# Performance work log

Measured on AMD Instinct MI355X. Metric: run time of the kernel, lower is better.

## Reference

```python
import jax, jax.numpy as jnp
import numpy as np

C_IN, C_HID, N_HEADS = 64, 8, 8
INF, EPS, LN_EPS = 1000000000.0, 1e-10, 1e-5


def setup_inputs() -> dict:
    key = jax.random.key(0)
    ks = jax.random.split(key, 8)
    B, S, R = 1, 2048, 512  # batch, n_seq, n_res
    m = jax.random.normal(ks[0], (B, S, R, C_IN), dtype=jnp.float32)
    mask = jnp.ones((B, S, R), dtype=jnp.float32)
    sc = 1.0 / np.sqrt(C_IN)
    return {
        "m": m,
        "mask": mask,
        "ln_w": jnp.ones((C_IN,), jnp.float32),
        "ln_b": jnp.zeros((C_IN,), jnp.float32),
        "wq": jax.random.normal(ks[1], (C_IN, N_HEADS * C_HID), jnp.float32) * sc,
        "wk": jax.random.normal(ks[2], (C_IN, C_HID), jnp.float32) * sc,
        "wv": jax.random.normal(ks[3], (C_IN, C_HID), jnp.float32) * sc,
        "wg": jax.random.normal(ks[4], (C_IN, N_HEADS * C_HID), jnp.float32) * sc,
        "bg": jnp.ones((N_HEADS * C_HID,), jnp.float32),  # gating bias init to 1
        "wo": jax.random.normal(ks[5], (N_HEADS * C_HID, C_IN), jnp.float32) * sc,
        "bo": jnp.zeros((C_IN,), jnp.float32),
    }


def _layernorm(x, w, b):
    mu = jnp.mean(x, axis=-1, keepdims=True)
    var = jnp.mean(jnp.square(x - mu), axis=-1, keepdims=True)
    return (x - mu) * jax.lax.rsqrt(var + LN_EPS) * w + b


def reference(m, mask, ln_w, ln_b, wq, wk, wv, wg, bg, wo, bo):
    # m: [B, S, R, C]; attend over the MSA (S) axis per residue column.
    x = jnp.swapaxes(m, -2, -3)        # [B, R, S, C]
    msk = jnp.swapaxes(mask, -1, -2)   # [B, R, S]
    x = _layernorm(x, ln_w, ln_b)

    # mean-pooled query over the sequence axis
    q_pool = jnp.sum(x * msk[..., None], axis=-2) / (
        jnp.sum(msk, axis=-1)[..., None] + EPS)           # [B, R, C]
    q = (q_pool @ wq) * (C_HID ** -0.5)                    # [B, R, H*Ch]
    q = q.reshape(*q.shape[:-1], N_HEADS, C_HID)           # [B, R, H, Ch]

    k = x @ wk                                             # [B, R, S, Ch]
    v = x @ wv                                             # [B, R, S, Ch]

    bias = INF * (msk - 1.0)                               # [B, R, S]
    logits = jnp.einsum('brhc,brsc->brhs', q, k) + bias[..., None, :]
    a = jax.nn.softmax(logits, axis=-1)                    # [B, R, H, S]
    o = jnp.einsum('brhs,brsc->brhc', a, v)                # [B, R, H, Ch]

    g = jax.nn.sigmoid(x @ wg + bg)                        # [B, R, S, H*Ch]
    g = g.reshape(*g.shape[:-1], N_HEADS, C_HID)           # [B, R, S, H, Ch]
    o = o[..., None, :, :] * g                             # [B, R, S, H, Ch]
    o = o.reshape(*o.shape[:-2], N_HEADS * C_HID)          # [B, R, S, H*Ch]
    out = o @ wo + bo                                      # [B, R, S, C]
    return jnp.swapaxes(out, -2, -3)                       # [B, S, R, C]
```

## Files before the change

### kernel.cpp

```cpp
#include <hip/hip_runtime.h>
#include <hip/hip_bf16.h>

#define S_DIM 2048
#define R_DIM 512
#define C_DIM 64
#define LN_EPSF 1e-5f
#define EPSF 1e-10f
#define INFF 1000000000.0f

typedef __attribute__((ext_vector_type(4))) float f32x4;
typedef __attribute__((ext_vector_type(8))) short bf16x8;

__device__ __forceinline__ int SWZ(int row, int cb) {
  return row * 128 + (cb ^ ((row & 7) << 4));
}

__device__ __forceinline__ float wave_sum64(float v) {
#pragma unroll
  for (int m = 1; m < 64; m <<= 1) v += __shfl_xor(v, m, 64);
  return v;
}

__device__ __forceinline__ float bf2f(unsigned short u) {
  return __uint_as_float(((unsigned int)u) << 16);
}

__global__ __launch_bounds__(256) void kW(const float* __restrict__ wg,
                                          const float* __restrict__ wo,
                                          __hip_bfloat16* __restrict__ wgT,
                                          __hip_bfloat16* __restrict__ woT) {
  const float* src = blockIdx.x ? wo : wg;
  __hip_bfloat16* dst = blockIdx.x ? woT : wgT;
  for (int idx = threadIdx.x; idx < 4096; idx += 256) {
    const int n = idx >> 6, k = idx & 63;
    dst[idx] = __float2bfloat16(src[k * 64 + n]);
  }
}

template <bool STORE_X>
__global__ __launch_bounds__(256) void kA(
    const float* __restrict__ m_in, const float* __restrict__ mask,
    const float* __restrict__ ln_w, const float* __restrict__ ln_b,
    const float* __restrict__ wk, const float* __restrict__ wv,
    __hip_bfloat16* __restrict__ x_ws, __hip_bfloat16* __restrict__ k_ws,
    __hip_bfloat16* __restrict__ v_ws, float* __restrict__ qnum,
    float* __restrict__ msum) {
  const int tid = threadIdx.x;
  const int w = tid >> 6;
  const int lane = tid & 63;
  const int r = blockIdx.x & (R_DIM - 1);
  const int chunk = blockIdx.x >> 9;
  const int s_base = chunk * 32;

  const float lw = ln_w[lane];
  const float lb = ln_b[lane];

  const int j = lane & 15;
  const int q4 = lane >> 4;
  const int jj = j & 7;
  const float* wmat = (j < 8) ? wk : wv;
  float wreg[16];
#pragma unroll
  for (int cc = 0; cc < 16; ++cc) wreg[cc] = wmat[(q4 * 16 + cc) * 8 + jj];

  float qacc = 0.f;
  float macc = 0.f;

  for (int it = 0; it < 8; ++it) {
    const int s = s_base + it * 4 + w;
    const size_t pos = (size_t)s * R_DIM + r;
    const float xv = m_in[pos * 64 + lane];
    const float mk = mask[pos];
    const float mu = wave_sum64(xv) * (1.f / 64.f);
    const float d = xv - mu;
    const float var = wave_sum64(d * d) * (1.f / 64.f);
    const float xn = fmaf(d * rsqrtf(var + LN_EPSF), lw, lb);

    qacc = fmaf(xn, mk, qacc);
    macc += mk;

    if (STORE_X) x_ws[pos * 64 + lane] = __float2bfloat16(xn);

    float acc = 0.f;
#pragma unroll
    for (int cc = 0; cc < 16; ++cc) {
      const float xc = __shfl(xn, q4 * 16 + cc, 64);
      acc = fmaf(xc, wreg[cc], acc);
    }
    acc += __shfl_xor(acc, 16, 64);
    acc += __shfl_xor(acc, 32, 64);
    if (lane < 16) {
      const __hip_bfloat16 hb = __float2bfloat16(acc);
      const size_t kvb = ((size_t)r * S_DIM + s) * 8 + jj;
      if (lane < 8) k_ws[kvb] = hb; else v_ws[kvb] = hb;
    }
  }

  __shared__ float qsm[4][64];
  __shared__ float mssm[4];
  qsm[w][lane] = qacc;
  if (lane == 0) mssm[w] = macc;
  __syncthreads();
  if (w == 0) {
    const float t = qsm[0][lane] + qsm[1][lane] + qsm[2][lane] + qsm[3][lane];
    atomicAdd(&qnum[r * 64 + lane], t);
    if (lane == 0) atomicAdd(&msum[r], mssm[0] + mssm[1] + mssm[2] + mssm[3]);
  }
}

__global__ __launch_bounds__(256) void kB(
    const float* __restrict__ qnum, const float* __restrict__ msum,
    const float* __restrict__ mask, const float* __restrict__ wq,
    const __hip_bfloat16* __restrict__ k_ws,
    const __hip_bfloat16* __restrict__ v_ws, float* __restrict__ o_ws) {
  const int r = blockIdx.x;
  const int tid = threadIdx.x;
  __shared__ float qp_sm[64];
  __shared__ float q_sm[64];
  if (tid < 64) qp_sm[tid] = qnum[r * 64 + tid] / (msum[r] + EPSF);
  __syncthreads();
  if (tid < 64) {
    float a = 0.f;
#pragma unroll
    for (int c = 0; c < 64; ++c) a = fmaf(qp_sm[c], wq[c * 64 + tid], a);
    q_sm[tid] = a * 0.35355339059327373f;
  }
  __syncthreads();

  const int w = tid >> 6;
  const int lane = tid & 63;
  const int h0 = w * 2;
  float qh0[8], qh1[8];
#pragma unroll
  for (int ch = 0; ch < 8; ++ch) {
    qh0[ch] = q_sm[h0 * 8 + ch];
    qh1[ch] = q_sm[h0 * 8 + 8 + ch];
  }
  float m0 = -1e30f, l0 = 0.f, m1 = -1e30f, l1 = 0.f;
  float a0[8], a1[8];
#pragma unroll
  for (int ch = 0; ch < 8; ++ch) { a0[ch] = 0.f; a1[ch] = 0.f; }

  for (int it = 0; it < 32; ++it) {
    const int s = it * 64 + lane;
    const size_t kb = ((size_t)r * S_DIM + s) * 8;
    union { uint4 u; unsigned short us[8]; } ku, vu;
    ku.u = *reinterpret_cast<const uint4*>(&k_ws[kb]);
    vu.u = *reinterpret_cast<const uint4*>(&v_ws[kb]);
    const float bias = INFF * (mask[(size_t)s * R_DIM + r] - 1.f);
    float lg0 = bias, lg1 = bias;
#pragma unroll
    for (int ch = 0; ch < 8; ++ch) {
      const float kc = bf2f(ku.us[ch]);
      lg0 = fmaf(qh0[ch], kc, lg0);
      lg1 = fmaf(qh1[ch], kc, lg1);
    }
    const float nm0 = fmaxf(m0, lg0);
    const float c0 = __expf(m0 - nm0);
    const float p0 = __expf(lg0 - nm0);
    const float nm1 = fmaxf(m1, lg1);
    const float c1 = __expf(m1 - nm1);
    const float p1 = __expf(lg1 - nm1);
    l0 = fmaf(l0, c0, p0); m0 = nm0;
    l1 = fmaf(l1, c1, p1); m1 = nm1;
#pragma unroll
    for (int ch = 0; ch < 8; ++ch) {
      const float vc = bf2f(vu.us[ch]);
      a0[ch] = fmaf(a0[ch], c0, p0 * vc);
      a1[ch] = fmaf(a1[ch], c1, p1 * vc);
    }
  }
#pragma unroll
  for (int msk = 1; msk < 64; msk <<= 1) {
    {
      const float om = __shfl_xor(m0, msk, 64);
      const float ol = __shfl_xor(l0, msk, 64);
      const float nm = fmaxf(m0, om);
      const float ca = __expf(m0 - nm);
      const float cb = __expf(om - nm);
      l0 = l0 * ca + ol * cb;
#pragma unroll
      for (int ch = 0; ch < 8; ++ch) {
        const float oa = __shfl_xor(a0[ch], msk, 64);
        a0[ch] = a0[ch] * ca + oa * cb;
      }
      m0 = nm;
    }
    {
      const float om = __shfl_xor(m1, msk, 64);
      const float ol = __shfl_xor(l1, msk, 64);
      const float nm = fmaxf(m1, om);
      const float ca = __expf(m1 - nm);
      const float cb = __expf(om - nm);
      l1 = l1 * ca + ol * cb;
#pragma unroll
      for (int ch = 0; ch < 8; ++ch) {
        const float oa = __shfl_xor(a1[ch], msk, 64);
        a1[ch] = a1[ch] * ca + oa * cb;
      }
      m1 = nm;
    }
  }
  const float inv0 = 1.f / l0;
  const float inv1 = 1.f / l1;
#pragma unroll
  for (int ch = 0; ch < 8; ++ch) {
    if (lane == ch)     o_ws[r * 64 + h0 * 8 + ch]       = a0[ch] * inv0;
    if (lane == 8 + ch) o_ws[r * 64 + (h0 + 1) * 8 + ch] = a1[ch] * inv1;
  }
}

__global__ __launch_bounds__(256) void kC_mfma(
    const __hip_bfloat16* __restrict__ x_ws, const float* __restrict__ o_ws,
    const __hip_bfloat16* __restrict__ wgT, const __hip_bfloat16* __restrict__ woT,
    const float* __restrict__ bg, const float* __restrict__ bo,
    float* __restrict__ out) {
  __shared__ __align__(16) unsigned char smem[32768];
  unsigned char* xsm  = smem;
  unsigned char* wg_s = smem + 16384;
  unsigned char* wo_s = smem + 24576;
  const int t = threadIdx.x;
  const int w = t >> 6;
  const int l = t & 63;
  const size_t P0 = (size_t)blockIdx.x * 128;

  {
    const uint4* sg = (const uint4*)wgT;
    const uint4* so = (const uint4*)woT;
#pragma unroll
    for (int pp = 0; pp < 2; ++pp) {
      const int idx = pp * 256 + t;
      const int row = idx >> 3;
      const int cb = (idx & 7) * 16;
      *(uint4*)(wg_s + SWZ(row, cb)) = sg[idx];
      *(uint4*)(wo_s + SWZ(row, cb)) = so[idx];
    }
  }
  {
    const uint4* sx = (const uint4*)(x_ws + P0 * 64);
#pragma unroll
    for (int pp = 0; pp < 4; ++pp) {
      const int idx = pp * 256 + t;
      const int row = idx >> 3;
      const int cb = (idx & 7) * 16;
      *(uint4*)(xsm + SWZ(row, cb)) = sx[idx];
    }
  }
  __syncthreads();

  const int woff = w * 32;
  const int lrow = l & 15;
  const int g16 = l >> 4;

  f32x4 acc[2][4] = {};
#pragma unroll
  for (int ks = 0; ks < 2; ++ks) {
    bf16x8 a[2], b[4];
#pragma unroll
    for (int mb = 0; mb < 2; ++mb)
      a[mb] = *(const bf16x8*)(xsm + SWZ(woff + mb * 16 + lrow, ks * 64 + g16 * 16));
#pragma unroll
    for (int nb = 0; nb < 4; ++nb)
      b[nb] = *(const bf16x8*)(wg_s + SWZ(nb * 16 + lrow, ks * 64 + g16 * 16));
#pragma unroll
    for (int mb = 0; mb < 2; ++mb)
#pragma unroll
      for (int nb = 0; nb < 4; ++nb)
        acc[mb][nb] = __builtin_amdgcn_mfma_f32_16x16x32_bf16(a[mb], b[nb], acc[mb][nb], 0, 0, 0);
  }
  __syncthreads();

  const int r0 = (int)(P0 & (R_DIM - 1));
#pragma unroll
  for (int nb = 0; nb < 4; ++nb) {
    const int col = nb * 16 + lrow;
    const float bgv = bg[col];
#pragma unroll
    for (int mb = 0; mb < 2; ++mb) {
#pragma unroll
      for (int i = 0; i < 4; ++i) {
        const int row = woff + mb * 16 + g16 * 4 + i;
        const float gv = 1.f / (1.f + __expf(-(acc[mb][nb][i] + bgv)));
        const float og = gv * o_ws[(r0 + row) * 64 + col];
        *(__hip_bfloat16*)(xsm + SWZ(row, col * 2)) = __float2bfloat16(og);
      }
    }
  }
  __syncthreads();

  f32x4 acc2[2][4] = {};
#pragma unroll
  for (int ks = 0; ks < 2; ++ks) {
    bf16x8 a[2], b[4];
#pragma unroll
    for (int mb = 0; mb < 2; ++mb)
      a[mb] = *(const bf16x8*)(xsm + SWZ(woff + mb * 16 + lrow, ks * 64 + g16 * 16));
#pragma unroll
    for (int nb = 0; nb < 4; ++nb)
      b[nb] = *(const bf16x8*)(wo_s + SWZ(nb * 16 + lrow, ks * 64 + g16 * 16));
#pragma unroll
    for (int mb = 0; mb < 2; ++mb)
#pragma unroll
      for (int nb = 0; nb < 4; ++nb)
        acc2[mb][nb] = __builtin_amdgcn_mfma_f32_16x16x32_bf16(a[mb], b[nb], acc2[mb][nb], 0, 0, 0);
  }

#pragma unroll
  for (int nb = 0; nb < 4; ++nb) {
    const int col = nb * 16 + lrow;
    const float bov = bo[col];
#pragma unroll
    for (int mb = 0; mb < 2; ++mb)
#pragma unroll
      for (int i = 0; i < 4; ++i) {
        const int row = woff + mb * 16 + g16 * 4 + i;
        out[(P0 + row) * 64 + col] = acc2[mb][nb][i] + bov;
      }
  }
}

template <bool USE_X>
__global__ __launch_bounds__(256) void kC(
    const __hip_bfloat16* __restrict__ x_ws, const float* __restrict__ m_in,
    const float* __restrict__ ln_w, const float* __restrict__ ln_b,
    const float* __restrict__ o_ws, const float* __restrict__ wg,
    const float* __restrict__ bg, const float* __restrict__ wo,
    const float* __restrict__ bo, float* __restrict__ out) {
  const int tid = threadIdx.x;
  const int w = tid >> 6;
  const int lane = tid & 63;
  const size_t p0 = ((size_t)blockIdx.x * 4 + w) * 4;
  __shared__ float xsm[4][4][64];
  __shared__ float ogsm[4][4][64];

  if (USE_X) {
#pragma unroll
    for (int pp = 0; pp < 4; ++pp)
      xsm[w][pp][lane] = __bfloat162float(x_ws[(p0 + pp) * 64 + lane]);
  } else {
    const float lw = ln_w[lane];
    const float lb = ln_b[lane];
#pragma unroll
    for (int pp = 0; pp < 4; ++pp) {
      const float xv = m_in[(p0 + pp) * 64 + lane];
      const float mu = wave_sum64(xv) * (1.f / 64.f);
      const float d = xv - mu;
      const float var = wave_sum64(d * d) * (1.f / 64.f);
      xsm[w][pp][lane] = fmaf(d * rsqrtf(var + LN_EPSF), lw, lb);
    }
  }
  __syncthreads();

  float acc[4];
  const float bgv = bg[lane];
#pragma unroll
  for (int pp = 0; pp < 4; ++pp) acc[pp] = bgv;
#pragma unroll 4
  for (int c4 = 0; c4 < 16; ++c4) {
    const float wv0 = wg[(c4 * 4 + 0) * 64 + lane];
    const float wv1 = wg[(c4 * 4 + 1) * 64 + lane];
    const float wv2 = wg[(c4 * 4 + 2) * 64 + lane];
    const float wv3 = wg[(c4 * 4 + 3) * 64 + lane];
#pragma unroll
    for (int pp = 0; pp < 4; ++pp) {
      const float4 xq = *reinterpret_cast<const float4*>(&xsm[w][pp][c4 * 4]);
      acc[pp] = fmaf(xq.x, wv0, acc[pp]);
      acc[pp] = fmaf(xq.y, wv1, acc[pp]);
      acc[pp] = fmaf(xq.z, wv2, acc[pp]);
      acc[pp] = fmaf(xq.w, wv3, acc[pp]);
    }
  }
  const int rr = (int)(p0 & (R_DIM - 1));
#pragma unroll
  for (int pp = 0; pp < 4; ++pp) {
    const float g = 1.f / (1.f + __expf(-acc[pp]));
    ogsm[w][pp][lane] = g * o_ws[(rr + pp) * 64 + lane];
  }
  __syncthreads();

  float acc2[4];
  const float bov = bo[lane];
#pragma unroll
  for (int pp = 0; pp < 4; ++pp) acc2[pp] = bov;
#pragma unroll 4
  for (int j4 = 0; j4 < 16; ++j4) {
    const float wv0 = wo[(j4 * 4 + 0) * 64 + lane];
    const float wv1 = wo[(j4 * 4 + 1) * 64 + lane];
    const float wv2 = wo[(j4 * 4 + 2) * 64 + lane];
    const float wv3 = wo[(j4 * 4 + 3) * 64 + lane];
#pragma unroll
    for (int pp = 0; pp < 4; ++pp) {
      const float4 oq = *reinterpret_cast<const float4*>(&ogsm[w][pp][j4 * 4]);
      acc2[pp] = fmaf(oq.x, wv0, acc2[pp]);
      acc2[pp] = fmaf(oq.y, wv1, acc2[pp]);
      acc2[pp] = fmaf(oq.z, wv2, acc2[pp]);
      acc2[pp] = fmaf(oq.w, wv3, acc2[pp]);
    }
  }
#pragma unroll
  for (int pp = 0; pp < 4; ++pp) out[(p0 + pp) * 64 + lane] = acc2[pp];
}

extern "C" void kernel_launch(void* const* d_in, const int* in_sizes, int n_in,
                              void* d_out, int out_size, void* d_ws,
                              size_t ws_size, hipStream_t stream) {
  (void)in_sizes; (void)n_in; (void)out_size;
  const float* m_in = (const float*)d_in[0];
  const float* mask = (const float*)d_in[1];
  const float* ln_w = (const float*)d_in[2];
  const float* ln_b = (const float*)d_in[3];
  const float* wq   = (const float*)d_in[4];
  const float* wk   = (const float*)d_in[5];
  const float* wv   = (const float*)d_in[6];
  const float* wg   = (const float*)d_in[7];
  const float* bg   = (const float*)d_in[8];
  const float* wo   = (const float*)d_in[9];
  const float* bo   = (const float*)d_in[10];
  float* out = (float*)d_out;
  char* ws = (char*)d_ws;

  const size_t X_BYTES  = (size_t)S_DIM * R_DIM * 64 * 2;
  const size_t KV_BYTES = (size_t)S_DIM * R_DIM * 8 * 2;
  const size_t QN_BYTES = (size_t)R_DIM * 64 * 4;
  const size_t MS_BYTES = (size_t)R_DIM * 4;
  const size_t O_BYTES  = (size_t)R_DIM * 64 * 4;
  const size_t WT_BYTES = 64 * 64 * 2;

  const size_t need_big =
      X_BYTES + 2 * KV_BYTES + QN_BYTES + MS_BYTES + O_BYTES + 2 * WT_BYTES;
  const bool use_x = ws_size >= need_big;

  size_t off = use_x ? X_BYTES : 0;
  __hip_bfloat16* x_ws = (__hip_bfloat16*)ws;
  __hip_bfloat16* k_ws = (__hip_bfloat16*)(ws + off); off += KV_BYTES;
  __hip_bfloat16* v_ws = (__hip_bfloat16*)(ws + off); off += KV_BYTES;
  float* qnum = (float*)(ws + off); off += QN_BYTES;
  float* msum = (float*)(ws + off); off += MS_BYTES;
  float* o_ws = (float*)(ws + off); off += O_BYTES;
  __hip_bfloat16* wgT = (__hip_bfloat16*)(ws + off); off += WT_BYTES;
  __hip_bfloat16* woT = (__hip_bfloat16*)(ws + off);

  hipMemsetAsync(qnum, 0, QN_BYTES + MS_BYTES, stream);

  const int gridA = R_DIM * (S_DIM / 32);
  if (use_x) {
    kW<<<2, 256, 0, stream>>>(wg, wo, wgT, woT);
    kA<true><<<gridA, 256, 0, stream>>>(m_in, mask, ln_w, ln_b, wk, wv, x_ws,
                                        k_ws, v_ws, qnum, msum);
    kB<<<R_DIM, 256, 0, stream>>>(qnum, msum, mask, wq, k_ws, v_ws, o_ws);
    const int gridC = (S_DIM * R_DIM) / 128;
    kC_mfma<<<gridC, 256, 0, stream>>>(x_ws, o_ws, wgT, woT, bg, bo, out);
  } else {
    kA<false><<<gridA, 256, 0, stream>>>(m_in, mask, ln_w, ln_b, wk, wv, x_ws,
                                         k_ws, v_ws, qnum, msum);
    kB<<<R_DIM, 256, 0, stream>>>(qnum, msum, mask, wq, k_ws, v_ws, o_ws);
    const int gridC = (S_DIM * R_DIM) / 16;
    kC<false><<<gridC, 256, 0, stream>>>(nullptr, m_in, ln_w, ln_b, o_ws, wg,
                                         bg, wo, bo, out);
  }
}
```

Baseline: 829.1 us.

## Rewrite LayerNorm/KV projection kernel with MFMA and 32-residue tiles

Replaces the per-position wave-level LayerNorm and shuffle-based K/V projection with a new kernel in which each block handles a 32-residue by 32-sequence tile. Two threads share a row and hold 32 floats each, so the LN statistics need only one shuffle. The K/V projection now runs as bf16 MFMA on a swizzled LDS tile, with K/V outputs staged in LDS and written as contiguous 16-byte stores. Query-pool accumulation switches from per-block LDS reduction plus atomics to per-thread register accumulators with many more global atomics. This adds register pressure (launch bounds set to 3 blocks per CU) and a larger atomic count in exchange for vectorised loads, far fewer shuffles and coalesced writes.

```diff
diff --git a/kernel.cpp b/kernel.cpp
--- a/kernel.cpp
+++ b/kernel.cpp
@@ -27,13 +27,180 @@
 
 __global__ __launch_bounds__(256) void kW(const float* __restrict__ wg,
                                           const float* __restrict__ wo,
+                                          const float* __restrict__ wk,
+                                          const float* __restrict__ wv,
                                           __hip_bfloat16* __restrict__ wgT,
-                                          __hip_bfloat16* __restrict__ woT) {
-  const float* src = blockIdx.x ? wo : wg;
-  __hip_bfloat16* dst = blockIdx.x ? woT : wgT;
-  for (int idx = threadIdx.x; idx < 4096; idx += 256) {
-    const int n = idx >> 6, k = idx & 63;
-    dst[idx] = __float2bfloat16(src[k * 64 + n]);
+                                          __hip_bfloat16* __restrict__ woT,
+                                          __hip_bfloat16* __restrict__ wkvT) {
+  if (blockIdx.x < 2) {
+    const float* src = blockIdx.x ? wo : wg;
+    __hip_bfloat16* dst = blockIdx.x ? woT : wgT;
+    for (int idx = threadIdx.x; idx < 4096; idx += 256) {
+      const int n = idx >> 6, k = idx & 63;
+      dst[idx] = __float2bfloat16(src[k * 64 + n]);
+    }
+  } else {
+    for (int idx = threadIdx.x; idx < 1024; idx += 256) {
+      const int n = idx >> 6, c = idx & 63;
+      const float v = (n < 8) ? wk[c * 8 + n] : wv[c * 8 + (n - 8)];
+      wkvT[idx] = __float2bfloat16(v);
+    }
+  }
+}
+
+template <bool STORE_X>
+__global__ __launch_bounds__(256, 3) void kA2(
+    const float* __restrict__ m_in, const float* __restrict__ mask,
+    const float* __restrict__ ln_w, const float* __restrict__ ln_b,
+    const __hip_bfloat16* __restrict__ wkvT, __hip_bfloat16* __restrict__ x_ws,
+    __hip_bfloat16* __restrict__ k_ws, __hip_bfloat16* __restrict__ v_ws,
+    float* __restrict__ qnum, float* __restrict__ msum) {
+  __shared__ __align__(16) unsigned char xsm[16384];
+  __shared__ __align__(16) unsigned char wkv_s[2048];
+  __shared__ __align__(16) unsigned char kvb[32768];
+
+  const int t = threadIdx.x;
+  const int w = t >> 6;
+  const int l = t & 63;
+  const int row = (t >> 1) & 31;
+  const int half = t & 1;
+  const int r0 = (blockIdx.x & 15) * 32;
+  const int s0 = (blockIdx.x >> 4) * 32;
+
+  if (t < 128) {
+    const uint4* src = (const uint4*)wkvT;
+    *(uint4*)(wkv_s + SWZ(t >> 3, (t & 7) * 16)) = src[t];
+  }
+
+  float lw[32], lb[32];
+  {
+    const float4* pw = (const float4*)(ln_w + half * 32);
+    const float4* pb = (const float4*)(ln_b + half * 32);
+#pragma unroll
+    for (int k = 0; k < 8; ++k) {
+      const float4 a = pw[k], b = pb[k];
+      lw[k * 4 + 0] = a.x; lw[k * 4 + 1] = a.y; lw[k * 4 + 2] = a.z; lw[k * 4 + 3] = a.w;
+      lb[k * 4 + 0] = b.x; lb[k * 4 + 1] = b.y; lb[k * 4 + 2] = b.z; lb[k * 4 + 3] = b.w;
+    }
+  }
+
+  float qacc[32];
+#pragma unroll
+  for (int j = 0; j < 32; ++j) qacc[j] = 0.f;
+  float macc = 0.f;
+
+  const int lrow = l & 15;
+  const int g16 = l >> 4;
+  unsigned char* xtile = xsm + w * 4096;
+
+  __syncthreads();
+
+  for (int it = 0; it < 8; ++it) {
+    const int s = s0 + it * 4 + w;
+    const size_t pos = (size_t)s * R_DIM + r0 + row;
+
+    float x[32];
+    {
+      const float4* pm = (const float4*)(m_in + pos * 64 + half * 32);
+#pragma unroll
+      for (int k = 0; k < 8; ++k) {
+        const float4 v4 = pm[k];
+        x[k * 4 + 0] = v4.x; x[k * 4 + 1] = v4.y;
+        x[k * 4 + 2] = v4.z; x[k * 4 + 3] = v4.w;
+      }
+    }
+    const float mk = mask[pos];
+
+    float sum = 0.f, sq = 0.f;
+#pragma unroll
+    for (int j = 0; j < 32; ++j) {
+      sum += x[j];
+      sq = fmaf(x[j], x[j], sq);
+    }
+    sum += __shfl_xor(sum, 1, 64);
+    sq += __shfl_xor(sq, 1, 64);
+    const float mu = sum * (1.f / 64.f);
+    const float var = sq * (1.f / 64.f) - mu * mu;
+    const float rs = rsqrtf(var + LN_EPSF);
+    const float nbias = -mu * rs;
+
+    unsigned int pk[16];
+#pragma unroll
+    for (int j = 0; j < 16; ++j) {
+      const float xn0 = fmaf(fmaf(x[2 * j], rs, nbias), lw[2 * j], lb[2 * j]);
+      const float xn1 = fmaf(fmaf(x[2 * j + 1], rs, nbias), lw[2 * j + 1], lb[2 * j + 1]);
+      qacc[2 * j] = fmaf(xn0, mk, qacc[2 * j]);
+      qacc[2 * j + 1] = fmaf(xn1, mk, qacc[2 * j + 1]);
+      const unsigned u0 = __bfloat16_as_ushort(__float2bfloat16(xn0));
+      const unsigned u1 = __bfloat16_as_ushort(__float2bfloat16(xn1));
+      pk[j] = u0 | (u1 << 16);
+    }
+    macc += mk;
+
+    if (STORE_X) {
+      uint4* dst = (uint4*)(x_ws + pos * 64 + half * 32);
+      const uint4* s4 = (const uint4*)pk;
+#pragma unroll
+      for (int k = 0; k < 4; ++k) dst[k] = s4[k];
+    }
+
+    {
+      const uint4* s4 = (const uint4*)pk;
+#pragma unroll
+      for (int k = 0; k < 4; ++k)
+        *(uint4*)(xtile + SWZ(row, half * 64 + k * 16)) = s4[k];
+    }
+
+    {
+      f32x4 acc2[2] = {};
+#pragma unroll
+      for (int ks = 0; ks < 2; ++ks) {
+        const bf16x8 bfr = *(const bf16x8*)(wkv_s + SWZ(lrow, ks * 64 + g16 * 16));
+#pragma unroll
+        for (int mb = 0; mb < 2; ++mb) {
+          const bf16x8 afr =
+              *(const bf16x8*)(xtile + SWZ(mb * 16 + lrow, ks * 64 + g16 * 16));
+          acc2[mb] =
+              __builtin_amdgcn_mfma_f32_16x16x32_bf16(afr, bfr, acc2[mb], 0, 0, 0);
+        }
+      }
+      const int sidx = it * 4 + w;
+      const int p = lrow >> 3, ch = lrow & 7;
+#pragma unroll
+      for (int mb = 0; mb < 2; ++mb)
+#pragma unroll
+        for (int i = 0; i < 4; ++i) {
+          const int rr = mb * 16 + g16 * 4 + i;
+          const int sidx_sw = (sidx & ~7) | ((sidx & 7) ^ (rr & 7));
+          *(__hip_bfloat16*)(kvb + (((p * 32 + rr) * 32 + sidx_sw) * 8 + ch) * 2) =
+              __float2bfloat16(acc2[mb][i]);
+        }
+    }
+  }
+
+  __syncthreads();
+
+  {
+    const int p = t >> 7;
+    const int rr = (t >> 2) & 31;
+    const int sq = t & 3;
+    __hip_bfloat16* dst =
+        (p ? v_ws : k_ws) + ((size_t)(r0 + rr) * S_DIM + s0 + sq * 8) * 8;
+#pragma unroll
+    for (int k = 0; k < 8; ++k) {
+      const int sidx = sq * 8 + k;
+      const int sidx_sw = (sidx & ~7) | ((sidx & 7) ^ (rr & 7));
+      const uint4 val =
+          *(const uint4*)(kvb + ((p * 32 + rr) * 32 + sidx_sw) * 16);
+      *(uint4*)(dst + k * 8) = val;
+    }
+  }
+
+  {
+    float* q = qnum + (size_t)(r0 + row) * 64 + half * 32;
+#pragma unroll
+    for (int j = 0; j < 32; ++j) atomicAdd(q + j, qacc[j]);
+    if (half == 0) atomicAdd(&msum[r0 + row], macc);
   }
 }
 
@@ -52,8 +219,8 @@
   const int chunk = blockIdx.x >> 9;
   const int s_base = chunk * 32;
 
-  const float lw = ln_w[lane];
-  const float lb = ln_b[lane];
+  const float lwv = ln_w[lane];
+  const float lbv = ln_b[lane];
 
   const int j = lane & 15;
   const int q4 = lane >> 4;
@@ -74,7 +241,7 @@
     const float mu = wave_sum64(xv) * (1.f / 64.f);
     const float d = xv - mu;
     const float var = wave_sum64(d * d) * (1.f / 64.f);
-    const float xn = fmaf(d * rsqrtf(var + LN_EPSF), lw, lb);
+    const float xn = fmaf(d * rsqrtf(var + LN_EPSF), lwv, lbv);
 
     qacc = fmaf(xn, mk, qacc);
     macc += mk;
@@ -91,8 +258,8 @@
     acc += __shfl_xor(acc, 32, 64);
     if (lane < 16) {
       const __hip_bfloat16 hb = __float2bfloat16(acc);
-      const size_t kvb = ((size_t)r * S_DIM + s) * 8 + jj;
-      if (lane < 8) k_ws[kvb] = hb; else v_ws[kvb] = hb;
+      const size_t kvb2 = ((size_t)r * S_DIM + s) * 8 + jj;
+      if (lane < 8) k_ws[kvb2] = hb; else v_ws[kvb2] = hb;
     }
   }
 
@@ -102,8 +269,8 @@
   if (lane == 0) mssm[w] = macc;
   __syncthreads();
   if (w == 0) {
-    const float t = qsm[0][lane] + qsm[1][lane] + qsm[2][lane] + qsm[3][lane];
-    atomicAdd(&qnum[r * 64 + lane], t);
+    const float tt = qsm[0][lane] + qsm[1][lane] + qsm[2][lane] + qsm[3][lane];
+    atomicAdd(&qnum[r * 64 + lane], tt);
     if (lane == 0) atomicAdd(&msum[r], mssm[0] + mssm[1] + mssm[2] + mssm[3]);
   }
 }
@@ -338,15 +505,15 @@
     for (int pp = 0; pp < 4; ++pp)
       xsm[w][pp][lane] = __bfloat162float(x_ws[(p0 + pp) * 64 + lane]);
   } else {
-    const float lw = ln_w[lane];
-    const float lb = ln_b[lane];
+    const float lwv = ln_w[lane];
+    const float lbv = ln_b[lane];
 #pragma unroll
     for (int pp = 0; pp < 4; ++pp) {
       const float xv = m_in[(p0 + pp) * 64 + lane];
       const float mu = wave_sum64(xv) * (1.f / 64.f);
       const float d = xv - mu;
       const float var = wave_sum64(d * d) * (1.f / 64.f);
-      xsm[w][pp][lane] = fmaf(d * rsqrtf(var + LN_EPSF), lw, lb);
+      xsm[w][pp][lane] = fmaf(d * rsqrtf(var + LN_EPSF), lwv, lbv);
     }
   }
   __syncthreads();
@@ -419,15 +586,16 @@
   float* out = (float*)d_out;
   char* ws = (char*)d_ws;
 
-  const size_t X_BYTES  = (size_t)S_DIM * R_DIM * 64 * 2;
-  const size_t KV_BYTES = (size_t)S_DIM * R_DIM * 8 * 2;
-  const size_t QN_BYTES = (size_t)R_DIM * 64 * 4;
-  const size_t MS_BYTES = (size_t)R_DIM * 4;
-  const size_t O_BYTES  = (size_t)R_DIM * 64 * 4;
-  const size_t WT_BYTES = 64 * 64 * 2;
-
-  const size_t need_big =
-      X_BYTES + 2 * KV_BYTES + QN_BYTES + MS_BYTES + O_BYTES + 2 * WT_BYTES;
+  const size_t X_BYTES   = (size_t)S_DIM * R_DIM * 64 * 2;
+  const size_t KV_BYTES  = (size_t)S_DIM * R_DIM * 8 * 2;
+  const size_t QN_BYTES  = (size_t)R_DIM * 64 * 4;
+  const size_t MS_BYTES  = (size_t)R_DIM * 4;
+  const size_t O_BYTES   = (size_t)R_DIM * 64 * 4;
+  const size_t WT_BYTES  = 64 * 64 * 2;
+  const size_t WKV_BYTES = 16 * 64 * 2;
+
+  const size_t need_big = X_BYTES + 2 * KV_BYTES + QN_BYTES + MS_BYTES +
+                          O_BYTES + 2 * WT_BYTES + WKV_BYTES;
   const bool use_x = ws_size >= need_big;
 
   size_t off = use_x ? X_BYTES : 0;
@@ -437,25 +605,25 @@
   float* qnum = (float*)(ws + off); off += QN_BYTES;
   float* msum = (float*)(ws + off); off += MS_BYTES;
   float* o_ws = (float*)(ws + off); off += O_BYTES;
-  __hip_bfloat16* wgT = (__hip_bfloat16*)(ws + off); off += WT_BYTES;
-  __hip_bfloat16* woT = (__hip_bfloat16*)(ws + off);
+  __hip_bfloat16* wgT  = (__hip_bfloat16*)(ws + off); off += WT_BYTES;
+  __hip_bfloat16* woT  = (__hip_bfloat16*)(ws + off); off += WT_BYTES;
+  __hip_bfloat16* wkvT = (__hip_bfloat16*)(ws + off);
 
   hipMemsetAsync(qnum, 0, QN_BYTES + MS_BYTES, stream);
 
-  const int gridA = R_DIM * (S_DIM / 32);
   if (use_x) {
-    kW<<<2, 256, 0, stream>>>(wg, wo, wgT, woT);
-    kA<true><<<gridA, 256, 0, stream>>>(m_in, mask, ln_w, ln_b, wk, wv, x_ws,
+    kW<<<3, 256, 0, stream>>>(wg, wo, wk, wv, wgT, woT, wkvT);
+    kA2<true><<<1024, 256, 0, stream>>>(m_in, mask, ln_w, ln_b, wkvT, x_ws,
                                         k_ws, v_ws, qnum, msum);
     kB<<<R_DIM, 256, 0, stream>>>(qnum, msum, mask, wq, k_ws, v_ws, o_ws);
-    const int gridC = (S_DIM * R_DIM) / 128;
-    kC_mfma<<<gridC, 256, 0, stream>>>(x_ws, o_ws, wgT, woT, bg, bo, out);
+    kC_mfma<<<(S_DIM * R_DIM) / 128, 256, 0, stream>>>(x_ws, o_ws, wgT, woT,
+                                                       bg, bo, out);
   } else {
+    const int gridA = R_DIM * (S_DIM / 32);
     kA<false><<<gridA, 256, 0, stream>>>(m_in, mask, ln_w, ln_b, wk, wv, x_ws,
                                          k_ws, v_ws, qnum, msum);
     kB<<<R_DIM, 256, 0, stream>>>(qnum, msum, mask, wq, k_ws, v_ws, o_ws);
-    const int gridC = (S_DIM * R_DIM) / 16;
-    kC<false><<<gridC, 256, 0, stream>>>(nullptr, m_in, ln_w, ln_b, o_ws, wg,
-                                         bg, wo, bo, out);
-  }
-}
+    kC<false><<<(S_DIM * R_DIM) / 16, 256, 0, stream>>>(
+        nullptr, m_in, ln_w, ln_b, o_ws, wg, bg, wo, bo, out);
+  }
+}
```

Measured after the change: 1.030 ms. 1.24x slower.
